# Kernel tuning notes

Measured on AMD Instinct MI355X. Metric: run time of the kernel, lower is better.

## Reference

```python
import jax, jax.numpy as jnp
import numpy as np

_EPS = 1e-08
SEG = 1024
HOP = 256
PAD = SEG // 2

# periodic Hann window, matching torch.hann_window(SEG) (periodic=True default)
_WINDOW = 0.5 * (1.0 - np.cos(2.0 * np.pi * np.arange(SEG) / SEG))


def setup_inputs() -> dict:
    key = jax.random.key(0)
    k1, k2 = jax.random.split(key)
    B, T = 32, 480000
    estimate = jax.random.normal(k1, (B, T), dtype=jnp.float32)
    target = jax.random.normal(k2, (B, T), dtype=jnp.float32)
    return {"estimate": estimate, "target": target}


def _frame(x):
    # x: [B, T_padded] -> [B, n_frames, SEG] overlapping frames (hop=HOP)
    n_frames = (x.shape[1] - SEG) // HOP + 1
    idx = np.arange(n_frames)[:, None] * HOP + np.arange(SEG)[None, :]
    return x[:, idx]


def reference(estimate, target):
    # zero-mean per utterance
    tgt = target - jnp.mean(target, axis=1, keepdims=True)
    est = estimate - jnp.mean(estimate, axis=1, keepdims=True)
    # centering: reflect-pad SEG//2 on both sides
    tgt = jnp.pad(tgt, ((0, 0), (PAD, PAD)), mode="reflect")
    est = jnp.pad(est, ((0, 0), (PAD, PAD)), mode="reflect")
    # overlapping frames + Hann windowing
    w = jnp.asarray(_WINDOW, dtype=tgt.dtype)  # [SEG]
    T_f = _frame(tgt) * w  # [B, F, SEG]
    E_f = _frame(est) * w  # [B, F, SEG]
    # SI-SDR per segment
    dot = jnp.sum(E_f * T_f, axis=2, keepdims=True)
    s_target_energy = jnp.sum(T_f * T_f, axis=2, keepdims=True) + _EPS
    scaled_target = dot * T_f / s_target_energy
    e_noise = E_f - scaled_target
    ratio = jnp.sum(scaled_target * scaled_target, axis=2) / (
        jnp.sum(e_noise * e_noise, axis=2) + _EPS
    )
    losses = -10.0 * jnp.log10(ratio + _EPS)  # [B, F]
    return losses
```

## Files before the change

### kernel.cpp

```cpp
#include <hip/hip_runtime.h>
#include <stdint.h>

#define NB 32
#define TLEN 480000
#define NF 1876
#define NCH 118
#define CH_F4 1216
#define WTHREADS 256

template <int CTRL>
__device__ __forceinline__ float dpp_add(float x) {
    int y = __builtin_amdgcn_update_dpp(0, __float_as_int(x), CTRL, 0xF, 0xF, true);
    return x + __int_as_float(y);
}

__device__ __forceinline__ float wave_reduce(float s) {
    s = dpp_add<0xB1>(s);
    s = dpp_add<0x4E>(s);
    s = dpp_add<0x124>(s);
    s = dpp_add<0x128>(s);
    s += __shfl_xor(s, 16);
    s += __shfl_xor(s, 32);
    return s;
}

__device__ __forceinline__ float f4c(const float4& v, int j) {
    return j == 0 ? v.x : (j == 1 ? v.y : (j == 2 ? v.z : v.w));
}

__device__ __forceinline__ float w2fast(float p) {
    float w = 0.5f - 0.5f * __cosf(p * (6.28318530717958647692f / 1024.0f));
    return w * w;
}

__device__ __forceinline__ void gl_lds16(const float4* gsrc, float4* ldst) {
    auto lds = reinterpret_cast<__attribute__((address_space(3))) uint32_t*>(
        reinterpret_cast<uintptr_t>(ldst));
    auto g = reinterpret_cast<const __attribute__((address_space(1))) uint32_t*>(
        reinterpret_cast<uintptr_t>(gsrc));
    __builtin_amdgcn_global_load_lds(g, lds, 16, 0, 0);
}

__global__ __launch_bounds__(WTHREADS) void seg_frames(
    const float* __restrict__ est, const float* __restrict__ tgt,
    float* __restrict__ ws_part, float* __restrict__ ws_bs)
{
    __shared__ float4 se4[CH_F4];
    __shared__ float4 st4[CH_F4];

    const int tid  = threadIdx.x;
    const int lane = tid & 63;
    const int wave = tid >> 6;
    const int b    = blockIdx.y;
    const int c    = blockIdx.x;

    const float* erow = est + (size_t)b * TLEN;
    const float* trow = tgt + (size_t)b * TLEN;

    if (c >= 1 && c <= 116) {
        const float4* e4 = (const float4*)erow;
        const float4* t4 = (const float4*)trow;
        const int g0 = 1024 * c - 128;
#pragma unroll
        for (int k = 0; k < 5; ++k) {
            int vb = k * 256 + 64 * wave;
            if (vb < CH_F4) {
                gl_lds16(&e4[g0 + vb + lane], &se4[vb]);
                gl_lds16(&t4[g0 + vb + lane], &st4[vb]);
            }
        }
    } else {
        float* se = (float*)se4;
        float* st = (float*)st4;
        for (int v = tid; v < 4 * CH_F4; v += WTHREADS) {
            int s = 4096 * c - 512 + v;
            int idx = s < 0 ? -s : (s >= TLEN ? 2 * (TLEN - 1) - s : s);
            se[v] = erow[idx];
            st[v] = trow[idx];
        }
    }
    __syncthreads();

    int owned = TLEN - 4096 * c;
    if (owned > 4096) owned = 4096;
    const int o4 = owned >> 2;
    float pe = 0.f, pt = 0.f;
    for (int u = tid; u < o4; u += WTHREADS) {
        float4 ev = se4[128 + u], tv = st4[128 + u];
        pe += (ev.x + ev.y) + (ev.z + ev.w);
        pt += (tv.x + tv.y) + (tv.z + tv.w);
    }
    pe = wave_reduce(pe);
    pt = wave_reduce(pt);
    if (lane == 0) {
        ws_bs[(0 * NB + b) * (NCH * 4) + c * 4 + wave] = pe;
        ws_bs[(1 * NB + b) * (NCH * 4) + c * 4 + wave] = pt;
    }

    int nfr = NF - 16 * c;
    if (nfr > 16) nfr = 16;
    if (4 * wave < nfr) {
        float w2v[4][4];
#pragma unroll
        for (int q = 0; q < 4; ++q)
#pragma unroll
            for (int j = 0; j < 4; ++j)
                w2v[q][j] = w2fast((float)(256 * q + 4 * lane + j));

        float acc[4][5];
#pragma unroll
        for (int i = 0; i < 4; ++i)
#pragma unroll
            for (int s5 = 0; s5 < 5; ++s5) acc[i][s5] = 0.f;

#pragma unroll
        for (int m = 0; m < 7; ++m) {
            float4 ev4 = se4[256 * wave + 64 * m + lane];
            float4 tv4 = st4[256 * wave + 64 * m + lane];
#pragma unroll
            for (int j = 0; j < 4; ++j) {
                float e = f4c(ev4, j), t = f4c(tv4, j);
                float et = e * t, tt2 = t * t, ee2 = e * e;
#pragma unroll
                for (int i = 0; i < 4; ++i) {
                    if (m - i < 0 || m - i > 3) continue;
                    float w2 = w2v[m - i][j];
                    acc[i][0] = fmaf(w2, et,  acc[i][0]);
                    acc[i][1] = fmaf(w2, tt2, acc[i][1]);
                    acc[i][2] = fmaf(w2, ee2, acc[i][2]);
                    acc[i][3] = fmaf(w2, e,   acc[i][3]);
                    acc[i][4] = fmaf(w2, t,   acc[i][4]);
                }
            }
        }

        const int f0 = 16 * c + 4 * wave;
        const int nlocal = (nfr - 4 * wave < 4) ? (nfr - 4 * wave) : 4;
#pragma unroll
        for (int i = 0; i < 4; ++i) {
            if (i < nlocal) {
                float s0 = wave_reduce(acc[i][0]);
                float s1 = wave_reduce(acc[i][1]);
                float s2 = wave_reduce(acc[i][2]);
                float s3 = wave_reduce(acc[i][3]);
                float s4 = wave_reduce(acc[i][4]);
                if (lane == 0) {
                    float* p = ws_part + (size_t)(b * NF + f0 + i) * 5;
                    p[0] = s0; p[1] = s1; p[2] = s2; p[3] = s3; p[4] = s4;
                }
            }
        }
    }
}

__global__ __launch_bounds__(WTHREADS) void seg_final(
    const float* __restrict__ ws_part, const float* __restrict__ ws_bs,
    float* __restrict__ out)
{
    const int tid  = threadIdx.x;
    const int lane = tid & 63;
    const int wave = tid >> 6;
    const int idx0 = blockIdx.x * WTHREADS;

    int b0 = idx0 / NF;
    int ilast = idx0 + WTHREADS - 1;
    if (ilast > NB * NF - 1) ilast = NB * NF - 1;
    int b1 = ilast / NF;

    __shared__ float smean[4];
    {
        int sig = wave & 1;
        int row = (wave >> 1) ? b1 : b0;
        const float* pbs = ws_bs + (size_t)(sig * NB + row) * (NCH * 4);
        float s = 0.f;
        for (int u = lane; u < NCH * 4; u += 64) s += pbs[u];
        s = wave_reduce(s);
        if (lane == 0) smean[wave] = s * (1.0f / (float)TLEN);
    }
    __syncthreads();

    int idx = idx0 + tid;
    if (idx >= NB * NF) return;
    int b = idx / NF;
    int which = (b == b0) ? 0 : 1;
    float me = smean[which * 2 + 0];
    float mt = smean[which * 2 + 1];

    const float* p = ws_part + (size_t)idx * 5;
    float S_et = p[0], S_tt = p[1], S_ee = p[2], S_e = p[3], S_t = p[4];
    const float W2 = 384.0f;

    float dot = S_et - mt * S_e - me * S_t + me * mt * W2;
    float tt  = S_tt - 2.0f * mt * S_t + mt * mt * W2;
    float ee  = S_ee - 2.0f * me * S_e + me * me * W2;

    float a     = dot / (tt + 1e-8f);
    float st2   = a * a * tt;
    float en2   = ee - 2.0f * a * dot + st2;
    float ratio = st2 / (en2 + 1e-8f);
    out[idx] = -10.0f * log10f(ratio + 1e-8f);
}

extern "C" void kernel_launch(void* const* d_in, const int* in_sizes, int n_in,
                              void* d_out, int out_size, void* d_ws, size_t ws_size,
                              hipStream_t stream)
{
    const float* est = (const float*)d_in[0];
    const float* tgt = (const float*)d_in[1];
    float* out = (float*)d_out;

    float* ws      = (float*)d_ws;
    float* ws_part = ws;
    float* ws_bs   = ws_part + (size_t)NB * NF * 5;

    dim3 grid1(NCH, NB);
    seg_frames<<<grid1, WTHREADS, 0, stream>>>(est, tgt, ws_part, ws_bs);
    dim3 grid2((NB * NF + WTHREADS - 1) / WTHREADS);
    seg_final<<<grid2, WTHREADS, 0, stream>>>(ws_part, ws_bs, out);
}
```

Before: 38.17 us.

## Process multiple smaller chunks per block with double-buffered LDS staging

Each block now walks a strip of 8 half-size chunks (8 frames each) instead of handling one 16-frame chunk. It double-buffers LDS so the async global-to-LDS load of the next chunk overlaps compute on the current one. The grid shrinks from 118 to 30 blocks per row, and the per-row mean partials shrink to match. The cost is a larger halo fraction per chunk, so more redundant loads (likely served by L2), and an extra barrier per chunk.

```diff
diff --git a/kernel.cpp b/kernel.cpp
--- a/kernel.cpp
+++ b/kernel.cpp
@@ -4,8 +4,10 @@
 #define NB 32
 #define TLEN 480000
 #define NF 1876
-#define NCH 118
-#define CH_F4 1216
+#define NCH 235
+#define CPB 8
+#define NSTRIP 30
+#define CH_F4 704
 #define WTHREADS 256
 
 template <int CTRL>
@@ -45,86 +47,85 @@
     const float* __restrict__ est, const float* __restrict__ tgt,
     float* __restrict__ ws_part, float* __restrict__ ws_bs)
 {
-    __shared__ float4 se4[CH_F4];
-    __shared__ float4 st4[CH_F4];
+    __shared__ float4 buf[2][2][CH_F4];
 
     const int tid  = threadIdx.x;
     const int lane = tid & 63;
     const int wave = tid >> 6;
     const int b    = blockIdx.y;
-    const int c    = blockIdx.x;
+    const int c0   = blockIdx.x * CPB;
 
     const float* erow = est + (size_t)b * TLEN;
     const float* trow = tgt + (size_t)b * TLEN;
-
-    if (c >= 1 && c <= 116) {
-        const float4* e4 = (const float4*)erow;
-        const float4* t4 = (const float4*)trow;
-        const int g0 = 1024 * c - 128;
-#pragma unroll
-        for (int k = 0; k < 5; ++k) {
-            int vb = k * 256 + 64 * wave;
-            if (vb < CH_F4) {
-                gl_lds16(&e4[g0 + vb + lane], &se4[vb]);
-                gl_lds16(&t4[g0 + vb + lane], &st4[vb]);
-            }
-        }
-    } else {
-        float* se = (float*)se4;
-        float* st = (float*)st4;
-        for (int v = tid; v < 4 * CH_F4; v += WTHREADS) {
-            int s = 4096 * c - 512 + v;
-            int idx = s < 0 ? -s : (s >= TLEN ? 2 * (TLEN - 1) - s : s);
-            se[v] = erow[idx];
-            st[v] = trow[idx];
-        }
-    }
+    const float4* e4 = (const float4*)erow;
+    const float4* t4 = (const float4*)trow;
+
+    auto stage = [&](int c, int d) {
+        if (c >= 1 && c <= 233) {
+            const int g0 = 512 * c - 128;
+#pragma unroll
+            for (int k = 0; k < 3; ++k) {
+                int vb = k * 256 + 64 * wave;
+                if (vb < CH_F4) {
+                    gl_lds16(&e4[g0 + vb + lane], &buf[d][0][vb]);
+                    gl_lds16(&t4[g0 + vb + lane], &buf[d][1][vb]);
+                }
+            }
+        } else {
+            float* se = (float*)&buf[d][0][0];
+            float* st = (float*)&buf[d][1][0];
+            for (int v = tid; v < 4 * CH_F4; v += WTHREADS) {
+                int s = 2048 * c - 512 + v;
+                int idx = s < 0 ? -s : (s >= TLEN ? 2 * (TLEN - 1) - s : s);
+                se[v] = erow[idx];
+                st[v] = trow[idx];
+            }
+        }
+    };
+
+    float w2v[4][4];
+#pragma unroll
+    for (int q = 0; q < 4; ++q)
+#pragma unroll
+        for (int j = 0; j < 4; ++j)
+            w2v[q][j] = w2fast((float)(256 * q + 4 * lane + j));
+
+    float pe = 0.f, pt = 0.f;
+
+    stage(c0, 0);
     __syncthreads();
 
-    int owned = TLEN - 4096 * c;
-    if (owned > 4096) owned = 4096;
-    const int o4 = owned >> 2;
-    float pe = 0.f, pt = 0.f;
-    for (int u = tid; u < o4; u += WTHREADS) {
-        float4 ev = se4[128 + u], tv = st4[128 + u];
-        pe += (ev.x + ev.y) + (ev.z + ev.w);
-        pt += (tv.x + tv.y) + (tv.z + tv.w);
-    }
-    pe = wave_reduce(pe);
-    pt = wave_reduce(pt);
-    if (lane == 0) {
-        ws_bs[(0 * NB + b) * (NCH * 4) + c * 4 + wave] = pe;
-        ws_bs[(1 * NB + b) * (NCH * 4) + c * 4 + wave] = pt;
-    }
-
-    int nfr = NF - 16 * c;
-    if (nfr > 16) nfr = 16;
-    if (4 * wave < nfr) {
-        float w2v[4][4];
-#pragma unroll
-        for (int q = 0; q < 4; ++q)
-#pragma unroll
-            for (int j = 0; j < 4; ++j)
-                w2v[q][j] = w2fast((float)(256 * q + 4 * lane + j));
-
-        float acc[4][5];
-#pragma unroll
-        for (int i = 0; i < 4; ++i)
+    for (int k = 0; k < CPB; ++k) {
+        const int c = c0 + k;
+        if (c >= NCH) break;
+        if (k + 1 < CPB && c + 1 < NCH) stage(c + 1, (k + 1) & 1);
+        const int d = k & 1;
+
+        const int owned4 = (c == NCH - 1) ? 192 : 512;
+        for (int u = tid; u < owned4; u += WTHREADS) {
+            float4 ev = buf[d][0][128 + u], tv = buf[d][1][128 + u];
+            pe += (ev.x + ev.y) + (ev.z + ev.w);
+            pt += (tv.x + tv.y) + (tv.z + tv.w);
+        }
+
+        float acc[2][5];
+#pragma unroll
+        for (int i = 0; i < 2; ++i)
 #pragma unroll
             for (int s5 = 0; s5 < 5; ++s5) acc[i][s5] = 0.f;
 
 #pragma unroll
-        for (int m = 0; m < 7; ++m) {
-            float4 ev4 = se4[256 * wave + 64 * m + lane];
-            float4 tv4 = st4[256 * wave + 64 * m + lane];
+        for (int mm = 0; mm < 5; ++mm) {
+            float4 ev4 = buf[d][0][(2 * wave + mm) * 64 + lane];
+            float4 tv4 = buf[d][1][(2 * wave + mm) * 64 + lane];
 #pragma unroll
             for (int j = 0; j < 4; ++j) {
                 float e = f4c(ev4, j), t = f4c(tv4, j);
                 float et = e * t, tt2 = t * t, ee2 = e * e;
 #pragma unroll
-                for (int i = 0; i < 4; ++i) {
-                    if (m - i < 0 || m - i > 3) continue;
-                    float w2 = w2v[m - i][j];
+                for (int i = 0; i < 2; ++i) {
+                    if (mm - i < 0 || mm - i > 3) continue;
+                    float w2 = w2v[mm - i][j];
                     acc[i][0] = fmaf(w2, et,  acc[i][0]);
                     acc[i][1] = fmaf(w2, tt2, acc[i][1]);
                     acc[i][2] = fmaf(w2, ee2, acc[i][2]);
@@ -134,22 +135,30 @@
             }
         }
 
-        const int f0 = 16 * c + 4 * wave;
-        const int nlocal = (nfr - 4 * wave < 4) ? (nfr - 4 * wave) : 4;
-#pragma unroll
-        for (int i = 0; i < 4; ++i) {
-            if (i < nlocal) {
+#pragma unroll
+        for (int i = 0; i < 2; ++i) {
+            int f = 8 * c + 2 * wave + i;
+            if (f < NF) {
                 float s0 = wave_reduce(acc[i][0]);
                 float s1 = wave_reduce(acc[i][1]);
                 float s2 = wave_reduce(acc[i][2]);
                 float s3 = wave_reduce(acc[i][3]);
                 float s4 = wave_reduce(acc[i][4]);
                 if (lane == 0) {
-                    float* p = ws_part + (size_t)(b * NF + f0 + i) * 5;
+                    float* p = ws_part + (size_t)(b * NF + f) * 5;
                     p[0] = s0; p[1] = s1; p[2] = s2; p[3] = s3; p[4] = s4;
                 }
             }
         }
+
+        __syncthreads();
+    }
+
+    pe = wave_reduce(pe);
+    pt = wave_reduce(pt);
+    if (lane == 0) {
+        ws_bs[(0 * NB + b) * (NSTRIP * 4) + blockIdx.x * 4 + wave] = pe;
+        ws_bs[(1 * NB + b) * (NSTRIP * 4) + blockIdx.x * 4 + wave] = pt;
     }
 }
 
@@ -171,9 +180,9 @@
     {
         int sig = wave & 1;
         int row = (wave >> 1) ? b1 : b0;
-        const float* pbs = ws_bs + (size_t)(sig * NB + row) * (NCH * 4);
+        const float* pbs = ws_bs + (size_t)(sig * NB + row) * (NSTRIP * 4);
         float s = 0.f;
-        for (int u = lane; u < NCH * 4; u += 64) s += pbs[u];
+        for (int u = lane; u < NSTRIP * 4; u += 64) s += pbs[u];
         s = wave_reduce(s);
         if (lane == 0) smean[wave] = s * (1.0f / (float)TLEN);
     }
@@ -213,7 +222,7 @@
     float* ws_part = ws;
     float* ws_bs   = ws_part + (size_t)NB * NF * 5;
 
-    dim3 grid1(NCH, NB);
+    dim3 grid1(NSTRIP, NB);
     seg_frames<<<grid1, WTHREADS, 0, stream>>>(est, tgt, ws_part, ws_bs);
     dim3 grid2((NB * NF + WTHREADS - 1) / WTHREADS);
     seg_final<<<grid2, WTHREADS, 0, stream>>>(ws_part, ws_bs, out);
```

Measured after the change: 44.04 us. 15.4% more time.
